# Kernel tuning notes

Measured on AMD Instinct MI355X. Metric: run time of the kernel, lower is better.

## Reference

```python
import jax, jax.numpy as jnp
import numpy as np

B, L, S, D, H, E, UV = 4, 2048, 2048, 1024, 8, 128, 128
ROT_DIM = H * E  # RotaryEmbedding(dim=qk_size*n_heads) applied on flattened dim


def gelu(x):
    return jax.nn.gelu(x, approximate=False)  # torch nn.GELU default (erf)


def rope(x):
    # x: [B, T, ROT_DIM]; interleaved-pair rotary (lucidrains rotary_embedding_torch default)
    T = x.shape[1]
    inv_freq = 1.0 / (10000.0 ** (jnp.arange(0, ROT_DIM, 2, dtype=jnp.float32) / ROT_DIM))
    freqs = jnp.arange(T, dtype=jnp.float32)[:, None] * inv_freq  # [T, ROT_DIM/2]
    cos = jnp.repeat(jnp.cos(freqs), 2, axis=-1)  # [T, ROT_DIM]
    sin = jnp.repeat(jnp.sin(freqs), 2, axis=-1)
    xp = x.reshape(*x.shape[:-1], ROT_DIM // 2, 2)
    x_rot = jnp.stack([-xp[..., 1], xp[..., 0]], axis=-1).reshape(x.shape)
    return x * cos + x_rot * sin


def setup_inputs() -> dict:
    key = jax.random.key(0)
    ks = jax.random.split(key, 16)
    n = lambda k, sh, s=1.0: jax.random.normal(k, sh, jnp.float32) * s
    w = 0.02
    return {
        "u": n(ks[0], (B, L, D)),
        "queries": n(ks[1], (B, L, D)),
        "keys": n(ks[2], (B, S, D)),
        "values": n(ks[3], (B, S, D)),
        "Wqk": n(ks[4], (D, H * E), w), "bqk": jnp.zeros((H * E,), jnp.float32),
        "Wv": n(ks[5], (D, H * UV), w), "bv": jnp.zeros((H * UV,), jnp.float32),
        "Wu": n(ks[6], (D, H * UV), w), "bu": jnp.zeros((H * UV,), jnp.float32),
        "Wo": n(ks[7], (H * UV, D), w), "bo": jnp.zeros((D,), jnp.float32),
        "q_gamma": jnp.ones((E,), jnp.float32), "q_beta": n(ks[8], (E,), w),
        "k_gamma": jnp.ones((E,), jnp.float32), "k_beta": n(ks[9], (E,), w),
    }


def _forward(u, queries, keys, values, Wqk, bqk, Wv, bv, Wu, bu, Wo, bo,
             q_gamma, q_beta, k_gamma, k_beta):
    # use_aff=True: shared qk projection + per-branch ScaleOffset over qk_size
    qk = gelu(queries @ Wqk + bqk)                      # [B,L,H*E]
    qk4 = qk.reshape(B, L, H, E)
    q = (qk4 * q_gamma + q_beta).reshape(B, L, H * E)
    k = (qk4 * k_gamma + k_beta).reshape(B, L, H * E)
    q = rope(q).reshape(B, L, H, E)
    k = rope(k).reshape(B, S, H, E)
    v = gelu(values @ Wv + bv).reshape(B, S, H, UV)
    # Conv1d(kernel_size=1) == pointwise linear over channels
    u_p = gelu(u @ Wu + bu).reshape(B, L, H, UV)
    scale = 1.0 / jnp.sqrt(jnp.float32(E))
    scores = jnp.einsum("blhe,bshe->bhls", q, k) * scale
    attn = jax.nn.softmax(scores, axis=-1)              # [B,H,L,S]
    ctx = jnp.einsum("bhls,bshd->blhd", attn, v)        # [B,L,H,UV]
    out = (u_p * ctx).reshape(B, L, H * UV)             # gate by u
    o = out @ Wo + bo                                   # [B,L,D]
    return o, attn


def reference(u, queries, keys, values, Wqk, bqk, Wv, bv, Wu, bu, Wo, bo,
              q_gamma, q_beta, k_gamma, k_beta):
    return _forward(u, queries, keys, values, Wqk, bqk, Wv, bv, Wu, bu, Wo, bo,
                    q_gamma, q_beta, k_gamma, k_beta)
```

## Files before the change

kernel.cpp:

```cpp
#include <hip/hip_runtime.h>
#include <hip/hip_bf16.h>
#include <math.h>

#define DEVI static __device__ __forceinline__

typedef __attribute__((ext_vector_type(4))) float f32x4;
typedef __attribute__((ext_vector_type(8))) short bf16x8;
typedef __attribute__((ext_vector_type(4))) short bf16x4;

constexpr int Bc = 4, Lc = 2048, Sc = 2048, Dc = 1024, Hc = 8, Ec = 128, UVc = 128;
constexpr int HEc = Hc * Ec;
constexpr int BLc = Bc * Lc;

DEVI unsigned f2bf_bits(float f) {
  unsigned u = __builtin_bit_cast(unsigned, f);
  return (u + 0x7FFFu + ((u >> 16) & 1u)) >> 16;
}
DEVI short f2bf(float f) { return (short)f2bf_bits(f); }
DEVI float bf2f(short s) {
  return __builtin_bit_cast(float, (unsigned)((unsigned short)s) << 16);
}
DEVI float gelu_f(float x) { return 0.5f * x * (1.0f + erff(x * 0.7071067811865476f)); }

DEVI void gload16(const void* gsrc, void* ldst) {
  __builtin_amdgcn_global_load_lds(
      (const __attribute__((address_space(1))) unsigned*)gsrc,
      (__attribute__((address_space(3))) unsigned*)(ldst), 16, 0, 0);
}

DEVI f32x4 mfma16(bf16x8 a, bf16x8 b, f32x4 c) {
  return __builtin_amdgcn_mfma_f32_16x16x32_bf16(a, b, c, 0, 0, 0);
}

__global__ void cvt_bf16_kernel(const float* __restrict__ in, short* __restrict__ out) {
  size_t i = ((size_t)blockIdx.x * 256 + threadIdx.x) * 8;
  float4 f1 = *reinterpret_cast<const float4*>(in + i);
  float4 f2 = *reinterpret_cast<const float4*>(in + i + 4);
  uint4 pk;
  pk.x = f2bf_bits(f1.x) | (f2bf_bits(f1.y) << 16);
  pk.y = f2bf_bits(f1.z) | (f2bf_bits(f1.w) << 16);
  pk.z = f2bf_bits(f2.x) | (f2bf_bits(f2.y) << 16);
  pk.w = f2bf_bits(f2.z) | (f2bf_bits(f2.w) << 16);
  *reinterpret_cast<uint4*>(out + i) = pk;
}

__global__ void wt_trans_kernel(const float* __restrict__ W0, const float* __restrict__ W1,
                                const float* __restrict__ W2, const float* __restrict__ W3,
                                short* __restrict__ T0, short* __restrict__ T1,
                                short* __restrict__ T2, short* __restrict__ T3) {
  __shared__ float t[32][33];
  const float* Ws[4] = {W0, W1, W2, W3};
  short* Ts[4] = {T0, T1, T2, T3};
  const float* W = Ws[blockIdx.z];
  short* WT = Ts[blockIdx.z];
  int tx = threadIdx.x, ty = threadIdx.y;
  int n0 = blockIdx.x * 32, k0 = blockIdx.y * 32;
#pragma unroll
  for (int i = 0; i < 4; i++) {
    int r = ty + i * 8;
    t[r][tx] = W[(size_t)(k0 + r) * 1024 + n0 + tx];
  }
  __syncthreads();
#pragma unroll
  for (int i = 0; i < 4; i++) {
    int r = ty + i * 8;
    WT[(size_t)(n0 + r) * 1024 + k0 + tx] = f2bf(t[tx][r]);
  }
}

__global__ void rope_cs_kernel(float2* __restrict__ cs) {
  int idx = blockIdx.x * 256 + threadIdx.x;
  int t = idx >> 9, i = idx & 511;
  float inv = expf((float)i * (-9.210340371976184f / 512.0f));
  float sv, cv;
  sincosf((float)t * inv, &sv, &cv);
  cs[idx] = make_float2(cv, sv);
}

template <int EPI>
__global__ __launch_bounds__(256, 3) void gemm_kernel(
    const short* __restrict__ A, const short* __restrict__ BT,
    const float* __restrict__ bias, void* __restrict__ Cptr, int M, int N, int K) {
  __shared__ char smem[49152];
  const int tid = threadIdx.x;
  const int wave = tid >> 6, lane = tid & 63;
  const int lquad = lane >> 4, l15 = lane & 15;
  const int m0 = blockIdx.x * 128, n0 = blockIdx.y * 128;
  const int wr = wave >> 1, wc = wave & 1;
  f32x4 acc[4][4] = {};

  const int q0 = tid * 16, q1 = tid * 16 + 4096;
  const int r0 = q0 >> 6, o0 = (q0 & 63) ^ ((r0 & 3) << 4);
  const int r1 = q1 >> 6, o1 = (q1 & 63) ^ ((r1 & 3) << 4);
  const short* a0 = A + (size_t)(m0 + r0) * K + (o0 >> 1);
  const short* a1 = A + (size_t)(m0 + r1) * K + (o1 >> 1);
  const short* b0 = BT + (size_t)(n0 + r0) * K + (o0 >> 1);
  const short* b1 = BT + (size_t)(n0 + r1) * K + (o1 >> 1);

#define G_STAGE(buf, kt)                     \
  {                                          \
    char* As_ = smem + (buf)*8192;           \
    char* Bs_ = smem + 24576 + (buf)*8192;   \
    gload16(a0 + (kt), As_ + q0);            \
    gload16(a1 + (kt), As_ + q1);            \
    gload16(b0 + (kt), Bs_ + q0);            \
    gload16(b1 + (kt), Bs_ + q1);            \
  }

  G_STAGE(0, 0);
  G_STAGE(1, 32);
  asm volatile("s_waitcnt vmcnt(4)" ::: "memory");
  __builtin_amdgcn_s_barrier();

  const int NT = K >> 5;
  int cur = 0;
  for (int t = 0; t < NT; t++) {
    int nb = cur + 2;
    if (nb >= 3) nb -= 3;
    G_STAGE(nb, (t + 2 < NT) ? (t + 2) * 32 : 0);
    __builtin_amdgcn_sched_barrier(0);
    const char* As_ = smem + cur * 8192;
    const char* Bs_ = smem + 24576 + cur * 8192;
    const int ko = lquad * 16;
    bf16x8 a[4], b[4];
#pragma unroll
    for (int f = 0; f < 4; f++) {
      int ra = wr * 64 + f * 16 + l15;
      a[f] = *reinterpret_cast<const bf16x8*>(As_ + ra * 64 + (ko ^ ((ra & 3) << 4)));
      int rb = wc * 64 + f * 16 + l15;
      b[f] = *reinterpret_cast<const bf16x8*>(Bs_ + rb * 64 + (ko ^ ((rb & 3) << 4)));
    }
#pragma unroll
    for (int mf = 0; mf < 4; mf++)
#pragma unroll
      for (int nf = 0; nf < 4; nf++)
        acc[mf][nf] = mfma16(a[mf], b[nf], acc[mf][nf]);
    asm volatile("s_waitcnt vmcnt(4) lgkmcnt(0)" ::: "memory");
    __builtin_amdgcn_sched_barrier(0);
    __builtin_amdgcn_s_barrier();
    cur = (cur == 2) ? 0 : cur + 1;
  }
#undef G_STAGE

#pragma unroll
  for (int mf = 0; mf < 4; mf++) {
#pragma unroll
    for (int nf = 0; nf < 4; nf++) {
      const int mrow = m0 + wr * 64 + mf * 16 + 4 * lquad;
      const int ncol = n0 + wc * 64 + nf * 16 + l15;
      const float bval = bias[ncol];
      if constexpr (EPI == 3) {
        int hh = ncol >> 7, dd = ncol & 127;
        int bb = mrow >> 11, ss = mrow & 2047;
        bf16x4 gv;
#pragma unroll
        for (int r = 0; r < 4; r++) gv[r] = f2bf(gelu_f(acc[mf][nf][r] + bval));
        *reinterpret_cast<bf16x4*>((short*)Cptr + (((size_t)bb * 8 + hh) * 128 + dd) * 2048 + ss) = gv;
      } else if constexpr (EPI == 1) {
#pragma unroll
        for (int r = 0; r < 4; r++)
          ((short*)Cptr)[(size_t)(mrow + r) * N + ncol] = f2bf(gelu_f(acc[mf][nf][r] + bval));
      } else {
#pragma unroll
        for (int r = 0; r < 4; r++)
          ((float*)Cptr)[(size_t)(mrow + r) * N + ncol] = acc[mf][nf][r] + bval;
      }
    }
  }
}

__global__ void rope_apply_kernel(const short* __restrict__ qkg,
                                  const float2* __restrict__ cstab,
                                  const float* __restrict__ qg, const float* __restrict__ qb,
                                  const float* __restrict__ kg, const float* __restrict__ kb,
                                  short* __restrict__ qo, short* __restrict__ ko) {
  int tid = blockIdx.x * 256 + threadIdx.x;
  size_t base = (size_t)tid * 8;
  int bl = (int)(base >> 10);
  int rem = (int)(base & 1023);
  int e0 = rem & 127;
  int t = bl & 2047;
  int pf = rem >> 1;
  uint4 raw = *reinterpret_cast<const uint4*>(qkg + base);
  short sh[8];
  *reinterpret_cast<uint4*>(sh) = raw;
  const float* csf = (const float*)cstab + (size_t)t * 1024 + 2 * pf;
  float4 p01 = *reinterpret_cast<const float4*>(csf);
  float4 p23 = *reinterpret_cast<const float4*>(csf + 4);
  float C[4] = {p01.x, p01.z, p23.x, p23.z};
  float Sn[4] = {p01.y, p01.w, p23.y, p23.w};
  float4 qga = *reinterpret_cast<const float4*>(qg + e0);
  float4 qgb = *reinterpret_cast<const float4*>(qg + e0 + 4);
  float4 qba = *reinterpret_cast<const float4*>(qb + e0);
  float4 qbb = *reinterpret_cast<const float4*>(qb + e0 + 4);
  float4 kga = *reinterpret_cast<const float4*>(kg + e0);
  float4 kgb = *reinterpret_cast<const float4*>(kg + e0 + 4);
  float4 kba = *reinterpret_cast<const float4*>(kb + e0);
  float4 kbb = *reinterpret_cast<const float4*>(kb + e0 + 4);
  float QG[8] = {qga.x, qga.y, qga.z, qga.w, qgb.x, qgb.y, qgb.z, qgb.w};
  float QB[8] = {qba.x, qba.y, qba.z, qba.w, qbb.x, qbb.y, qbb.z, qbb.w};
  float KG[8] = {kga.x, kga.y, kga.z, kga.w, kgb.x, kgb.y, kgb.z, kgb.w};
  float KB[8] = {kba.x, kba.y, kba.z, kba.w, kbb.x, kbb.y, kbb.z, kbb.w};
  short qsh[8], ksh[8];
#pragma unroll
  for (int j = 0; j < 4; j++) {
    float x0 = bf2f(sh[2 * j]), x1 = bf2f(sh[2 * j + 1]);
    float q0 = x0 * QG[2 * j] + QB[2 * j];
    float q1 = x1 * QG[2 * j + 1] + QB[2 * j + 1];
    qsh[2 * j] = f2bf(q0 * C[j] - q1 * Sn[j]);
    qsh[2 * j + 1] = f2bf(q1 * C[j] + q0 * Sn[j]);
    float k0v = x0 * KG[2 * j] + KB[2 * j];
    float k1v = x1 * KG[2 * j + 1] + KB[2 * j + 1];
    ksh[2 * j] = f2bf(k0v * C[j] - k1v * Sn[j]);
    ksh[2 * j + 1] = f2bf(k1v * C[j] + k0v * Sn[j]);
  }
  *reinterpret_cast<uint4*>(qo + base) = *reinterpret_cast<uint4*>(qsh);
  *reinterpret_cast<uint4*>(ko + base) = *reinterpret_cast<uint4*>(ksh);
}

__global__ __launch_bounds__(256, 3) void attn_kernel(
    const short* __restrict__ qs, const short* __restrict__ ks,
    const short* __restrict__ vT, const short* __restrict__ up,
    float* __restrict__ attn_out, short* __restrict__ gate) {
  __shared__ char smem[49152];
  const int bid = blockIdx.x;
  const int xcd = bid & 7, jj = bid >> 3;
  const int bh = xcd * 4 + (jj >> 5);
  const int lblk = jj & 31;
  const int b = bh >> 3, h = bh & 7;
  const int l0 = lblk * 64;
  const int tid = threadIdx.x;
  const int wave = tid >> 6, lane = tid & 63;
  const int lquad = lane >> 4, l15 = lane & 15;
  const float scale = 0.08838834764831845f;

  const short* ksrc[4];
  int kq[4];
#pragma unroll
  for (int i = 0; i < 4; i++) {
    int q = i * 4096 + tid * 16;
    kq[i] = q;
    int row = q >> 8, off = (q & 255) ^ ((row & 7) << 4);
    ksrc[i] = ks + (((size_t)b * Sc + row) * Hc + h) * Ec + (off >> 1);
  }
  const short* vsrc[2];
  int vq[2];
#pragma unroll
  for (int i = 0; i < 2; i++) {
    int q = i * 4096 + tid * 16;
    vq[i] = q;
    int rv = q >> 6;
    int j = (q >> 4) & 3;
    int c = (j - (rv & 3)) & 3;
    vsrc[i] = vT + ((size_t)bh * UVc + rv) * Sc + (c << 3);
  }

  bf16x8 qf[4];
  {
    int lrow = l0 + wave * 16 + l15;
    const short* qp = qs + (((size_t)b * Lc + lrow) * Hc + h) * Ec;
#pragma unroll
    for (int kt = 0; kt < 4; kt++)
      qf[kt] = *reinterpret_cast<const bf16x8*>(qp + kt * 32 + lquad * 8);
  }
  __builtin_amdgcn_sched_barrier(0);

#define STAGE_A(buf, s0)                                  \
  {                                                       \
    char* Kb_ = smem + (buf)*16384;                       \
    gload16(ksrc[0] + (size_t)(s0)*1024, Kb_ + kq[0]);    \
    gload16(ksrc[1] + (size_t)(s0)*1024, Kb_ + kq[1]);    \
    gload16(ksrc[2] + (size_t)(s0)*1024, Kb_ + kq[2]);    \
    gload16(ksrc[3] + (size_t)(s0)*1024, Kb_ + kq[3]);    \
  }

  STAGE_A(0, 0);
  STAGE_A(1, 64);
  asm volatile("s_waitcnt vmcnt(4)" ::: "memory");
  __builtin_amdgcn_s_barrier();
  float rsa = 0.f, rsb = 0.f;
  int cur = 0;
  for (int t = 0; t < 32; t++) {
    int nb = cur + 2;
    if (nb >= 3) nb -= 3;
    STAGE_A(nb, (t + 2 < 32) ? (t + 2) * 64 : 0);
    __builtin_amdgcn_sched_barrier(0);
    const char* KB_ = smem + cur * 16384;
    f32x4 d[4] = {};
    __builtin_amdgcn_s_setprio(1);
#pragma unroll
    for (int kt = 0; kt < 4; kt++)
#pragma unroll
      for (int sf = 0; sf < 4; sf++) {
        int row = sf * 16 + l15;
        bf16x8 kf = *reinterpret_cast<const bf16x8*>(
            KB_ + row * 256 + ((kt * 64 + lquad * 16) ^ ((row & 7) << 4)));
        d[sf] = mfma16(kf, qf[kt], d[sf]);
      }
    __builtin_amdgcn_s_setprio(0);
#pragma unroll
    for (int sf = 0; sf < 4; sf++)
#pragma unroll
      for (int r = 0; r < 4; r++) {
        float e = __expf(scale * d[sf][r]);
        if (sf & 1) rsb += e; else rsa += e;
      }
    asm volatile("s_waitcnt vmcnt(4) lgkmcnt(0)" ::: "memory");
    __builtin_amdgcn_sched_barrier(0);
    __builtin_amdgcn_s_barrier();
    cur = (cur == 2) ? 0 : cur + 1;
  }
#undef STAGE_A
  float rs = rsa + rsb;
  rs += __shfl_xor(rs, 16);
  rs += __shfl_xor(rs, 32);
  const float rcp = 1.0f / rs;

#define STAGE_B(buf, s0)                                  \
  {                                                       \
    char* Kb_ = smem + (buf)*8192;                        \
    char* Vb_ = smem + 24576 + (buf)*8192;                \
    gload16(ksrc[0] + (size_t)(s0)*1024, Kb_ + kq[0]);    \
    gload16(ksrc[1] + (size_t)(s0)*1024, Kb_ + kq[1]);    \
    gload16(vsrc[0] + (s0), Vb_ + vq[0]);                 \
    gload16(vsrc[1] + (s0), Vb_ + vq[1]);                 \
  }

  STAGE_B(0, 0);
  STAGE_B(1, 32);
  asm volatile("s_waitcnt vmcnt(4)" ::: "memory");
  __builtin_amdgcn_s_barrier();
  f32x4 ctx[8] = {};
  cur = 0;
  for (int t = 0; t < 64; t++) {
    const int s0 = t * 32;
    int nb = cur + 2;
    if (nb >= 3) nb -= 3;
    STAGE_B(nb, (t + 2 < 64) ? s0 + 64 : 0);
    __builtin_amdgcn_sched_barrier(0);
    const char* KB_ = smem + cur * 8192;
    const char* VB_ = smem + 24576 + cur * 8192;
    f32x4 d[2] = {};
    __builtin_amdgcn_s_setprio(1);
#pragma unroll
    for (int kt = 0; kt < 4; kt++)
#pragma unroll
      for (int sf = 0; sf < 2; sf++) {
        int row = sf * 16 + l15;
        bf16x8 kf = *reinterpret_cast<const bf16x8*>(
            KB_ + row * 256 + ((kt * 64 + lquad * 16) ^ ((row & 7) << 4)));
        d[sf] = mfma16(kf, qf[kt], d[sf]);
      }
    __builtin_amdgcn_s_setprio(0);
#pragma unroll
    for (int sf = 0; sf < 2; sf++)
#pragma unroll
      for (int r = 0; r < 4; r++)
        d[sf][r] = __expf(scale * d[sf][r]) * rcp;
    {
      int lrow = l0 + wave * 16 + l15;
      float* arow = attn_out + ((size_t)bh * Lc + lrow) * Sc + s0 + lquad * 4;
      __builtin_nontemporal_store(d[0], reinterpret_cast<f32x4*>(arow));
      __builtin_nontemporal_store(d[1], reinterpret_cast<f32x4*>(arow + 16));
    }
    bf16x8 pb;
#pragma unroll
    for (int r = 0; r < 4; r++) {
      pb[r] = f2bf(d[0][r]);
      pb[4 + r] = f2bf(d[1][r]);
    }
    __builtin_amdgcn_s_setprio(1);
#pragma unroll
    for (int df = 0; df < 8; df++) {
      int dd = df * 16 + l15;
      const char* vrow = VB_ + dd * 64;
      int half = (lquad & 1) * 8;
      int clo = ((lquad >> 1) + (dd & 3)) & 3;
      int chi = ((lquad >> 1) + 2 + (dd & 3)) & 3;
      bf16x4 lo = *reinterpret_cast<const bf16x4*>(vrow + clo * 16 + half);
      bf16x4 hi = *reinterpret_cast<const bf16x4*>(vrow + chi * 16 + half);
      bf16x8 vf = __builtin_shufflevector(lo, hi, 0, 1, 2, 3, 4, 5, 6, 7);
      ctx[df] = mfma16(vf, pb, ctx[df]);
    }
    __builtin_amdgcn_s_setprio(0);
    asm volatile("s_waitcnt vmcnt(6) lgkmcnt(0)" ::: "memory");
    __builtin_amdgcn_sched_barrier(0);
    __builtin_amdgcn_s_barrier();
    cur = (cur == 2) ? 0 : cur + 1;
  }
#undef STAGE_B

  {
    int lrow = l0 + wave * 16 + l15;
    size_t base = ((size_t)b * Lc + lrow) * HEc + h * UVc;
    const short* ub = up + base;
    short* gp = gate + base;
#pragma unroll
    for (int df = 0; df < 8; df++) {
      int doff = df * 16 + lquad * 4;
      bf16x4 uv = *reinterpret_cast<const bf16x4*>(ub + doff);
      bf16x4 gv;
#pragma unroll
      for (int r = 0; r < 4; r++)
        gv[r] = f2bf(bf2f(uv[r]) * ctx[df][r]);
      *reinterpret_cast<bf16x4*>(gp + doff) = gv;
    }
  }
}

extern "C" void kernel_launch(void* const* d_in, const int* in_sizes, int n_in,
                              void* d_out, int out_size, void* d_ws, size_t ws_size,
                              hipStream_t stream) {
  const float* u_in = (const float*)d_in[0];
  const float* qry = (const float*)d_in[1];
  const float* vals = (const float*)d_in[3];
  const float* Wqk = (const float*)d_in[4];
  const float* bqk = (const float*)d_in[5];
  const float* Wv = (const float*)d_in[6];
  const float* bv = (const float*)d_in[7];
  const float* Wu = (const float*)d_in[8];
  const float* bu = (const float*)d_in[9];
  const float* Wo = (const float*)d_in[10];
  const float* bo = (const float*)d_in[11];
  const float* qg = (const float*)d_in[12];
  const float* qb = (const float*)d_in[13];
  const float* kg = (const float*)d_in[14];
  const float* kb = (const float*)d_in[15];

  char* w = (char*)d_ws;
  short* WT0 = (short*)w; w += (size_t)1024 * 1024 * 2;
  short* WT1 = (short*)w; w += (size_t)1024 * 1024 * 2;
  short* WT2 = (short*)w; w += (size_t)1024 * 1024 * 2;
  short* WT3 = (short*)w; w += (size_t)1024 * 1024 * 2;
  float2* cstab = (float2*)w; w += (size_t)2048 * 512 * 8;
  const size_t BUF = (size_t)BLc * HEc * 2;
  short* C1 = (short*)w; w += BUF;
  short* C2 = (short*)w; w += BUF;
  short* C3 = (short*)w; w += BUF;
  short* qkg = (short*)w; w += BUF;
  short* qbf = (short*)w; w += BUF;
  short* vTb = (short*)w; w += BUF;
  short* upb = (short*)w; w += BUF;
  short* kbf = qkg;
  short* gtb = C1;

  float* o_out = (float*)d_out;
  float* attn_out = o_out + (size_t)BLc * Dc;

  dim3 tb(32, 8);
  cvt_bf16_kernel<<<4096, 256, 0, stream>>>(qry, C1);
  cvt_bf16_kernel<<<4096, 256, 0, stream>>>(vals, C2);
  cvt_bf16_kernel<<<4096, 256, 0, stream>>>(u_in, C3);
  wt_trans_kernel<<<dim3(32, 32, 4), tb, 0, stream>>>(Wqk, Wv, Wu, Wo, WT0, WT1, WT2, WT3);
  rope_cs_kernel<<<4096, 256, 0, stream>>>(cstab);

  gemm_kernel<1><<<dim3(64, 8), 256, 0, stream>>>(C1, WT0, bqk, qkg, BLc, HEc, Dc);
  rope_apply_kernel<<<4096, 256, 0, stream>>>(qkg, cstab, qg, qb, kg, kb, qbf, kbf);
  gemm_kernel<3><<<dim3(64, 8), 256, 0, stream>>>(C2, WT1, bv, vTb, BLc, HEc, Dc);
  gemm_kernel<1><<<dim3(64, 8), 256, 0, stream>>>(C3, WT2, bu, upb, BLc, HEc, Dc);
  attn_kernel<<<1024, 256, 0, stream>>>(qbf, kbf, vTb, upb, attn_out, gtb);
  gemm_kernel<0><<<dim3(64, 8), 256, 0, stream>>>(gtb, WT3, bo, o_out, BLc, Dc, HEc);
}
```

Baseline: 389.6 us.

## Split softmax row-sum pass into separate 32x32 MFMA kernel with folded exp2 scale

Moves the first attention pass (softmax denominators) out of attn_kernel into a new passa_kernel. That kernel uses 32x32x16 MFMA tiles over 128 query rows per block, which halves K-tile reloads per query row, and writes reciprocal row sums to a workspace buffer. The softmax scale and log2(e) are folded into q during RoPE so both passes use exp2f with no multiply. The three bf16 conversion launches are merged into one grid. The cost is an extra launch, a small global buffer round trip, and slightly different rounding because the scale is applied before the bf16 cast.

After: 390.4 us. Within noise of the previous version (+0.2%).

```diff
diff --git a/kernel.cpp b/kernel.cpp
--- a/kernel.cpp
+++ b/kernel.cpp
@@ -5,12 +5,15 @@
 #define DEVI static __device__ __forceinline__
 
 typedef __attribute__((ext_vector_type(4))) float f32x4;
+typedef __attribute__((ext_vector_type(16))) float f32x16;
 typedef __attribute__((ext_vector_type(8))) short bf16x8;
 typedef __attribute__((ext_vector_type(4))) short bf16x4;
 
 constexpr int Bc = 4, Lc = 2048, Sc = 2048, Dc = 1024, Hc = 8, Ec = 128, UVc = 128;
 constexpr int HEc = Hc * Ec;
 constexpr int BLc = Bc * Lc;
+
+#define QSC (1.44269504088896340f / 11.31370849898476039f)
 
 DEVI unsigned f2bf_bits(float f) {
   unsigned u = __builtin_bit_cast(unsigned, f);
@@ -31,8 +34,17 @@
 DEVI f32x4 mfma16(bf16x8 a, bf16x8 b, f32x4 c) {
   return __builtin_amdgcn_mfma_f32_16x16x32_bf16(a, b, c, 0, 0, 0);
 }
-
-__global__ void cvt_bf16_kernel(const float* __restrict__ in, short* __restrict__ out) {
+DEVI f32x16 mfma32(bf16x8 a, bf16x8 b, f32x16 c) {
+  return __builtin_amdgcn_mfma_f32_32x32x16_bf16(a, b, c, 0, 0, 0);
+}
+
+__global__ void cvt3_kernel(const float* __restrict__ i0, const float* __restrict__ i1,
+                            const float* __restrict__ i2, short* __restrict__ o0,
+                            short* __restrict__ o1, short* __restrict__ o2) {
+  const float* ins[3] = {i0, i1, i2};
+  short* outs[3] = {o0, o1, o2};
+  const float* in = ins[blockIdx.y];
+  short* out = outs[blockIdx.y];
   size_t i = ((size_t)blockIdx.x * 256 + threadIdx.x) * 8;
   float4 f1 = *reinterpret_cast<const float4*>(in + i);
   float4 f2 = *reinterpret_cast<const float4*>(in + i + 4);
@@ -207,8 +219,8 @@
     float x0 = bf2f(sh[2 * j]), x1 = bf2f(sh[2 * j + 1]);
     float q0 = x0 * QG[2 * j] + QB[2 * j];
     float q1 = x1 * QG[2 * j + 1] + QB[2 * j + 1];
-    qsh[2 * j] = f2bf(q0 * C[j] - q1 * Sn[j]);
-    qsh[2 * j + 1] = f2bf(q1 * C[j] + q0 * Sn[j]);
+    qsh[2 * j] = f2bf((q0 * C[j] - q1 * Sn[j]) * QSC);
+    qsh[2 * j + 1] = f2bf((q1 * C[j] + q0 * Sn[j]) * QSC);
     float k0v = x0 * KG[2 * j] + KB[2 * j];
     float k1v = x1 * KG[2 * j + 1] + KB[2 * j + 1];
     ksh[2 * j] = f2bf(k0v * C[j] - k1v * Sn[j]);
@@ -218,10 +230,97 @@
   *reinterpret_cast<uint4*>(ko + base) = *reinterpret_cast<uint4*>(ksh);
 }
 
+__global__ __launch_bounds__(256, 3) void passa_kernel(
+    const short* __restrict__ qs, const short* __restrict__ ks,
+    float* __restrict__ rcpbuf) {
+  __shared__ char smem[49152];
+  const int bid = blockIdx.x;
+  const int xcd = bid & 7, jj = bid >> 3;
+  const int bh = xcd * 4 + (jj >> 4);
+  const int lblk = jj & 15;
+  const int b = bh >> 3, h = bh & 7;
+  const int l0 = lblk * 128;
+  const int tid = threadIdx.x;
+  const int wave = tid >> 6, lane = tid & 63;
+  const int l31 = lane & 31, lhg = lane >> 5;
+
+  const short* ksrc[4];
+  int kq[4];
+#pragma unroll
+  for (int i = 0; i < 4; i++) {
+    int q = i * 4096 + tid * 16;
+    kq[i] = q;
+    int row = q >> 8, off = (q & 255) ^ ((row & 7) << 4);
+    ksrc[i] = ks + (((size_t)b * Sc + row) * Hc + h) * Ec + (off >> 1);
+  }
+
+  bf16x8 qf[8];
+  {
+    const char* qp = (const char*)(qs + (((size_t)b * Lc + l0 + wave * 32 + l31) * Hc + h) * Ec);
+#pragma unroll
+    for (int kt = 0; kt < 8; kt++)
+      qf[kt] = *reinterpret_cast<const bf16x8*>(qp + kt * 32 + 16 * lhg);
+  }
+  __builtin_amdgcn_sched_barrier(0);
+
+#define STAGE_A(buf, s0)                                  \
+  {                                                       \
+    char* Kb_ = smem + (buf)*16384;                       \
+    gload16(ksrc[0] + (size_t)(s0)*1024, Kb_ + kq[0]);    \
+    gload16(ksrc[1] + (size_t)(s0)*1024, Kb_ + kq[1]);    \
+    gload16(ksrc[2] + (size_t)(s0)*1024, Kb_ + kq[2]);    \
+    gload16(ksrc[3] + (size_t)(s0)*1024, Kb_ + kq[3]);    \
+  }
+
+  STAGE_A(0, 0);
+  STAGE_A(1, 64);
+  asm volatile("s_waitcnt vmcnt(4)" ::: "memory");
+  __builtin_amdgcn_s_barrier();
+  float ra = 0.f, rb = 0.f, rc = 0.f, rd = 0.f;
+  int cur = 0;
+  for (int t = 0; t < 32; t++) {
+    int nb = cur + 2;
+    if (nb >= 3) nb -= 3;
+    STAGE_A(nb, (t + 2 < 32) ? (t + 2) * 64 : 0);
+    __builtin_amdgcn_sched_barrier(0);
+    const char* KB_ = smem + cur * 16384;
+    f32x16 d0 = {}, d1 = {};
+    __builtin_amdgcn_s_setprio(1);
+#pragma unroll
+    for (int kt = 0; kt < 8; kt++) {
+      int row0 = l31, row1 = 32 + l31;
+      bf16x8 k0 = *reinterpret_cast<const bf16x8*>(
+          KB_ + row0 * 256 + ((kt * 32 + 16 * lhg) ^ ((row0 & 7) << 4)));
+      bf16x8 k1 = *reinterpret_cast<const bf16x8*>(
+          KB_ + row1 * 256 + ((kt * 32 + 16 * lhg) ^ ((row1 & 7) << 4)));
+      d0 = mfma32(k0, qf[kt], d0);
+      d1 = mfma32(k1, qf[kt], d1);
+    }
+    __builtin_amdgcn_s_setprio(0);
+#pragma unroll
+    for (int r = 0; r < 16; r += 4) {
+      ra += exp2f(d0[r]) + exp2f(d1[r]);
+      rb += exp2f(d0[r + 1]) + exp2f(d1[r + 1]);
+      rc += exp2f(d0[r + 2]) + exp2f(d1[r + 2]);
+      rd += exp2f(d0[r + 3]) + exp2f(d1[r + 3]);
+    }
+    asm volatile("s_waitcnt vmcnt(4) lgkmcnt(0)" ::: "memory");
+    __builtin_amdgcn_sched_barrier(0);
+    __builtin_amdgcn_s_barrier();
+    cur = (cur == 2) ? 0 : cur + 1;
+  }
+#undef STAGE_A
+  float rs = (ra + rb) + (rc + rd);
+  rs += __shfl_xor(rs, 32);
+  if (lane < 32)
+    rcpbuf[(size_t)bh * Lc + l0 + wave * 32 + l31] = 1.0f / rs;
+}
+
 __global__ __launch_bounds__(256, 3) void attn_kernel(
     const short* __restrict__ qs, const short* __restrict__ ks,
     const short* __restrict__ vT, const short* __restrict__ up,
-    float* __restrict__ attn_out, short* __restrict__ gate) {
+    const float* __restrict__ rcpbuf, float* __restrict__ attn_out,
+    short* __restrict__ gate) {
   __shared__ char smem[49152];
   const int bid = blockIdx.x;
   const int xcd = bid & 7, jj = bid >> 3;
@@ -232,12 +331,11 @@
   const int tid = threadIdx.x;
   const int wave = tid >> 6, lane = tid & 63;
   const int lquad = lane >> 4, l15 = lane & 15;
-  const float scale = 0.08838834764831845f;
-
-  const short* ksrc[4];
-  int kq[4];
-#pragma unroll
-  for (int i = 0; i < 4; i++) {
+
+  const short* ksrc[2];
+  int kq[2];
+#pragma unroll
+  for (int i = 0; i < 2; i++) {
     int q = i * 4096 + tid * 16;
     kq[i] = q;
     int row = q >> 8, off = (q & 255) ^ ((row & 7) << 4);
@@ -263,58 +361,8 @@
     for (int kt = 0; kt < 4; kt++)
       qf[kt] = *reinterpret_cast<const bf16x8*>(qp + kt * 32 + lquad * 8);
   }
+  const float rcp = rcpbuf[(size_t)bh * Lc + l0 + wave * 16 + l15];
   __builtin_amdgcn_sched_barrier(0);
-
-#define STAGE_A(buf, s0)                                  \
-  {                                                       \
-    char* Kb_ = smem + (buf)*16384;                       \
-    gload16(ksrc[0] + (size_t)(s0)*1024, Kb_ + kq[0]);    \
-    gload16(ksrc[1] + (size_t)(s0)*1024, Kb_ + kq[1]);    \
-    gload16(ksrc[2] + (size_t)(s0)*1024, Kb_ + kq[2]);    \
-    gload16(ksrc[3] + (size_t)(s0)*1024, Kb_ + kq[3]);    \
-  }
-
-  STAGE_A(0, 0);
-  STAGE_A(1, 64);
-  asm volatile("s_waitcnt vmcnt(4)" ::: "memory");
-  __builtin_amdgcn_s_barrier();
-  float rsa = 0.f, rsb = 0.f;
-  int cur = 0;
-  for (int t = 0; t < 32; t++) {
-    int nb = cur + 2;
-    if (nb >= 3) nb -= 3;
-    STAGE_A(nb, (t + 2 < 32) ? (t + 2) * 64 : 0);
-    __builtin_amdgcn_sched_barrier(0);
-    const char* KB_ = smem + cur * 16384;
-    f32x4 d[4] = {};
-    __builtin_amdgcn_s_setprio(1);
-#pragma unroll
-    for (int kt = 0; kt < 4; kt++)
-#pragma unroll
-      for (int sf = 0; sf < 4; sf++) {
-        int row = sf * 16 + l15;
-        bf16x8 kf = *reinterpret_cast<const bf16x8*>(
-            KB_ + row * 256 + ((kt * 64 + lquad * 16) ^ ((row & 7) << 4)));
-        d[sf] = mfma16(kf, qf[kt], d[sf]);
-      }
-    __builtin_amdgcn_s_setprio(0);
-#pragma unroll
-    for (int sf = 0; sf < 4; sf++)
-#pragma unroll
-      for (int r = 0; r < 4; r++) {
-        float e = __expf(scale * d[sf][r]);
-        if (sf & 1) rsb += e; else rsa += e;
-      }
-    asm volatile("s_waitcnt vmcnt(4) lgkmcnt(0)" ::: "memory");
-    __builtin_amdgcn_sched_barrier(0);
-    __builtin_amdgcn_s_barrier();
-    cur = (cur == 2) ? 0 : cur + 1;
-  }
-#undef STAGE_A
-  float rs = rsa + rsb;
-  rs += __shfl_xor(rs, 16);
-  rs += __shfl_xor(rs, 32);
-  const float rcp = 1.0f / rs;
 
 #define STAGE_B(buf, s0)                                  \
   {                                                       \
@@ -331,7 +379,7 @@
   asm volatile("s_waitcnt vmcnt(4)" ::: "memory");
   __builtin_amdgcn_s_barrier();
   f32x4 ctx[8] = {};
-  cur = 0;
+  int cur = 0;
   for (int t = 0; t < 64; t++) {
     const int s0 = t * 32;
     int nb = cur + 2;
@@ -356,7 +404,7 @@
     for (int sf = 0; sf < 2; sf++)
 #pragma unroll
       for (int r = 0; r < 4; r++)
-        d[sf][r] = __expf(scale * d[sf][r]) * rcp;
+        d[sf][r] = exp2f(d[sf][r]) * rcp;
     {
       int lrow = l0 + wave * 16 + l15;
       float* arow = attn_out + ((size_t)bh * Lc + lrow) * Sc + s0 + lquad * 4;
@@ -433,6 +481,7 @@
   short* WT2 = (short*)w; w += (size_t)1024 * 1024 * 2;
   short* WT3 = (short*)w; w += (size_t)1024 * 1024 * 2;
   float2* cstab = (float2*)w; w += (size_t)2048 * 512 * 8;
+  float* rcpb = (float*)w; w += (size_t)32 * 2048 * 4;
   const size_t BUF = (size_t)BLc * HEc * 2;
   short* C1 = (short*)w; w += BUF;
   short* C2 = (short*)w; w += BUF;
@@ -448,16 +497,15 @@
   float* attn_out = o_out + (size_t)BLc * Dc;
 
   dim3 tb(32, 8);
-  cvt_bf16_kernel<<<4096, 256, 0, stream>>>(qry, C1);
-  cvt_bf16_kernel<<<4096, 256, 0, stream>>>(vals, C2);
-  cvt_bf16_kernel<<<4096, 256, 0, stream>>>(u_in, C3);
+  cvt3_kernel<<<dim3(4096, 3), 256, 0, stream>>>(qry, vals, u_in, C1, C2, C3);
   wt_trans_kernel<<<dim3(32, 32, 4), tb, 0, stream>>>(Wqk, Wv, Wu, Wo, WT0, WT1, WT2, WT3);
   rope_cs_kernel<<<4096, 256, 0, stream>>>(cstab);
 
   gemm_kernel<1><<<dim3(64, 8), 256, 0, stream>>>(C1, WT0, bqk, qkg, BLc, HEc, Dc);
   rope_apply_kernel<<<4096, 256, 0, stream>>>(qkg, cstab, qg, qb, kg, kb, qbf, kbf);
+  passa_kernel<<<512, 256, 0, stream>>>(qbf, kbf, rcpb);
   gemm_kernel<3><<<dim3(64, 8), 256, 0, stream>>>(C2, WT1, bv, vTb, BLc, HEc, Dc);
   gemm_kernel<1><<<dim3(64, 8), 256, 0, stream>>>(C3, WT2, bu, upb, BLc, HEc, Dc);
-  attn_kernel<<<1024, 256, 0, stream>>>(qbf, kbf, vTb, upb, attn_out, gtb);
+  attn_kernel<<<1024, 256, 0, stream>>>(qbf, kbf, vTb, upb, rcpb, attn_out, gtb);
   gemm_kernel<0><<<dim3(64, 8), 256, 0, stream>>>(gtb, WT3, bo, o_out, BLc, Dc, HEc);
 }
```
